# Kernel optimization log

Measured on AMD Instinct MI355X. Metric: run time of the kernel, lower is better.

The kernel has to match this reference:

```python
import jax, jax.numpy as jnp
import numpy as np

E = 8            # num_experts
TOPK = 2
CAP_FACTOR = 1.0
MIN_CAP = 4
AUX_COEF = 0.01


def setup_inputs() -> dict:
    key = jax.random.key(0)
    k1, k2, k3, k4 = jax.random.split(key, 4)
    S, H, F = 2048, 1024, 4096
    return {
        "hidden_states": jax.random.normal(k1, (S, H), dtype=jnp.float32),
        "wg": jax.random.normal(k2, (H, E), dtype=jnp.float32) * 0.02,
        "w1": jax.random.normal(k3, (E, H, F), dtype=jnp.float32) * 0.02,
        "w2": jax.random.normal(k4, (E, F, H), dtype=jnp.float32) * 0.02,
    }


def reference(hidden_states, wg, w1, w2):
    x = hidden_states  # [S, H]
    S, H = x.shape
    capacity = max(int(np.ceil(S * TOPK * CAP_FACTOR / E)), MIN_CAP)  # static

    # ---- top-2 gating (DeepSpeed top2gating) ----
    logits = x @ wg                                   # [S, E]
    gates = jax.nn.softmax(logits, axis=-1)
    idx1 = jnp.argmax(gates, axis=1)
    mask1 = jax.nn.one_hot(idx1, E, dtype=x.dtype)    # [S, E]
    logits_wo1 = jnp.where(mask1 > 0, -jnp.inf, logits)
    idx2 = jnp.argmax(logits_wo1, axis=1)
    mask2 = jax.nn.one_hot(idx2, E, dtype=x.dtype)

    # positions within each expert buffer
    loc1 = jnp.cumsum(mask1, axis=0) - 1.0                      # [S, E]
    loc2 = jnp.cumsum(mask2, axis=0) - 1.0 + jnp.sum(mask1, axis=0, keepdims=True)

    # load-balancing aux loss (computed before capacity drop)
    me = jnp.mean(gates, axis=0)
    ce = jnp.mean(mask1, axis=0)
    l_aux = jnp.mean(me * ce) * E * E * AUX_COEF
    exp_counts = jnp.sum(mask1, axis=0).astype(jnp.int32)

    # drop tokens over capacity
    mask1 = mask1 * (loc1 < capacity).astype(x.dtype)
    mask2 = mask2 * (loc2 < capacity).astype(x.dtype)

    loc1_s = jnp.sum(loc1 * mask1, axis=1).astype(jnp.int32)    # [S]
    loc2_s = jnp.sum(loc2 * mask2, axis=1).astype(jnp.int32)

    gates1_s = jnp.sum(gates * mask1, axis=1)                   # [S]
    gates2_s = jnp.sum(gates * mask2, axis=1)
    denom = jnp.clip(gates1_s + gates2_s, jnp.finfo(x.dtype).eps, None)
    g1 = gates1_s / denom
    g2 = gates2_s / denom

    oh1 = jax.nn.one_hot(loc1_s, capacity, dtype=x.dtype)       # [S, C]
    oh2 = jax.nn.one_hot(loc2_s, capacity, dtype=x.dtype)
    combine = (g1[:, None, None] * mask1[:, :, None] * oh1[:, None, :]
               + g2[:, None, None] * mask2[:, :, None] * oh2[:, None, :])  # [S, E, C]
    dispatch_mask = (combine > 0).astype(x.dtype)

    # ---- dispatch, expert grouped-GEMM (MLP: gelu), combine ----
    dispatched = jnp.einsum("sec,sh->ech", dispatch_mask, x)    # [E, C, H]
    h = jax.nn.gelu(jnp.einsum("ech,ehf->ecf", dispatched, w1))
    expert_out = jnp.einsum("ecf,efh->ech", h, w2)              # [E, C, H]
    output = jnp.einsum("sec,ech->sh", combine, expert_out)     # [S, H]

    return output, l_aux, exp_counts
```

## Files before the change

### kernel.cpp

```cpp
#include <hip/hip_runtime.h>
#include <cstdint>
#include <cstddef>

#define NT 2048
#define HD 1024
#define FD 4096
#define NE 8
#define CAP 512

typedef __bf16 bf16x8_t __attribute__((ext_vector_type(8)));
typedef float f32x4_t __attribute__((ext_vector_type(4)));

typedef const __attribute__((address_space(1))) void* as1_cvp;
typedef __attribute__((address_space(3))) void* as3_vp;

__device__ __forceinline__ void load_lds16(const void* g, void* s) {
  __builtin_amdgcn_global_load_lds((as1_cvp)g, (as3_vp)s, 16, 0, 0);
}

__device__ __forceinline__ unsigned short f2bf(float f) {
  unsigned int u = __float_as_uint(f);
  unsigned int r = (u + 0x7fffu + ((u >> 16) & 1u)) >> 16;
  return (unsigned short)r;
}

__device__ __forceinline__ float gelu_tanh(float x) {
  float inner = 0.7978845608028654f * (x + 0.044715f * x * x * x);
  return 0.5f * x * (1.0f + tanhf(inner));
}

__global__ __launch_bounds__(64) void gating_kernel(
    const float* __restrict__ x, const float* __restrict__ wg,
    float* __restrict__ gates, int* __restrict__ idx1, int* __restrict__ idx2,
    float* __restrict__ gate1, float* __restrict__ gate2)
{
  int s = blockIdx.x;
  int lane = threadIdx.x;
  const float* xs = x + (size_t)s * HD;
  float acc[NE];
  #pragma unroll
  for (int e = 0; e < NE; ++e) acc[e] = 0.f;
  #pragma unroll
  for (int i = 0; i < HD / 64; ++i) {
    int h = i * 64 + lane;
    float xv = xs[h];
    const float4 w0 = *(const float4*)(wg + (size_t)h * NE);
    const float4 w1 = *(const float4*)(wg + (size_t)h * NE + 4);
    acc[0] += xv * w0.x; acc[1] += xv * w0.y; acc[2] += xv * w0.z; acc[3] += xv * w0.w;
    acc[4] += xv * w1.x; acc[5] += xv * w1.y; acc[6] += xv * w1.z; acc[7] += xv * w1.w;
  }
  #pragma unroll
  for (int off = 32; off > 0; off >>= 1) {
    #pragma unroll
    for (int e = 0; e < NE; ++e) acc[e] += __shfl_down(acc[e], off);
  }
  if (lane == 0) {
    float m = acc[0];
    #pragma unroll
    for (int e = 1; e < NE; ++e) m = fmaxf(m, acc[e]);
    float p[NE]; float sum = 0.f;
    #pragma unroll
    for (int e = 0; e < NE; ++e) { p[e] = expf(acc[e] - m); sum += p[e]; }
    float inv = 1.0f / sum;
    int i1 = 0; float b1 = acc[0];
    #pragma unroll
    for (int e = 1; e < NE; ++e) if (acc[e] > b1) { b1 = acc[e]; i1 = e; }
    int i2 = (i1 == 0) ? 1 : 0; float b2 = acc[i2];
    #pragma unroll
    for (int e = 0; e < NE; ++e) if (e != i1 && acc[e] > b2) { b2 = acc[e]; i2 = e; }
    #pragma unroll
    for (int e = 0; e < NE; ++e) gates[(size_t)s * NE + e] = p[e] * inv;
    idx1[s] = i1; idx2[s] = i2;
    gate1[s] = p[i1] * inv;
    gate2[s] = p[i2] * inv;
  }
}

__global__ __launch_bounds__(512) void scan_kernel(
    const int* __restrict__ idx1, const int* __restrict__ idx2,
    const float* __restrict__ gate1, const float* __restrict__ gate2,
    const float* __restrict__ gates,
    int* __restrict__ loc1a, int* __restrict__ loc2a,
    float* __restrict__ g1a, float* __restrict__ g2a,
    int* __restrict__ slot1a, int* __restrict__ slot2a,
    int* __restrict__ slot_tok, float* __restrict__ out_tail)
{
  __shared__ int cnt1[NE];
  __shared__ float gsum[NE];
  int tid = threadIdx.x;
  for (int i = tid; i < NE * CAP; i += 512) slot_tok[i] = -1;
  if (tid < NE) gsum[tid] = 0.f;
  int w = tid >> 6, lane = tid & 63;
  unsigned long long below = (1ull << lane) - 1ull;

  int run = 0;
  for (int c = 0; c < NT / 64; ++c) {
    int s = c * 64 + lane;
    bool m = (idx1[s] == w);
    unsigned long long bal = __ballot(m);
    if (m) loc1a[s] = run + (int)__popcll(bal & below);
    run += (int)__popcll(bal);
  }
  if (lane == 0) cnt1[w] = run;
  int run2 = run;
  for (int c = 0; c < NT / 64; ++c) {
    int s = c * 64 + lane;
    bool m = (idx2[s] == w);
    unsigned long long bal = __ballot(m);
    if (m) loc2a[s] = run2 + (int)__popcll(bal & below);
    run2 += (int)__popcll(bal);
  }
  __syncthreads();

  for (int s = tid; s < NT; s += 512) {
    int e1 = idx1[s], e2 = idx2[s];
    int l1 = loc1a[s], l2 = loc2a[s];
    bool k1 = (l1 < CAP), k2 = (l2 < CAP);
    float g1r = k1 ? gate1[s] : 0.f;
    float g2r = k2 ? gate2[s] : 0.f;
    float denom = fmaxf(g1r + g2r, 1.1920929e-07f);
    g1a[s] = g1r / denom;
    g2a[s] = g2r / denom;
    int s1 = k1 ? (e1 * CAP + l1) : -1;
    int s2 = k2 ? (e2 * CAP + l2) : -1;
    slot1a[s] = s1; slot2a[s] = s2;
    if (s1 >= 0) slot_tok[s1] = s;
    if (s2 >= 0) slot_tok[s2] = s;
  }

  float part[NE];
  #pragma unroll
  for (int e = 0; e < NE; ++e) part[e] = 0.f;
  for (int s = tid; s < NT; s += 512) {
    const float* gr = gates + (size_t)s * NE;
    #pragma unroll
    for (int e = 0; e < NE; ++e) part[e] += gr[e];
  }
  #pragma unroll
  for (int e = 0; e < NE; ++e) atomicAdd(&gsum[e], part[e]);
  __syncthreads();
  if (tid == 0) {
    float laux = 0.f;
    #pragma unroll
    for (int e = 0; e < NE; ++e)
      laux += (gsum[e] / (float)NT) * ((float)cnt1[e] / (float)NT);
    laux *= (float)(NE * NE) * 0.01f;
    out_tail[0] = laux;
  }
  if (tid < NE) out_tail[1 + tid] = (float)cnt1[tid];
}

__global__ __launch_bounds__(256) void transpose_cast_kernel(
    const float* __restrict__ in, unsigned short* __restrict__ out, int K, int N)
{
  __shared__ float tile[64 * 65];
  size_t ebase = (size_t)blockIdx.z * (size_t)K * N;
  const float* ine = in + ebase;
  unsigned short* oute = out + ebase;
  int n0 = blockIdx.x * 64, k0 = blockIdx.y * 64;
  int tid = threadIdx.x;
  #pragma unroll
  for (int i = 0; i < 4; ++i) {
    int chunk = i * 256 + tid;
    int r = chunk >> 4, c = (chunk & 15) * 4;
    float4 v = *(const float4*)(ine + (size_t)(k0 + r) * N + n0 + c);
    tile[r * 65 + c + 0] = v.x;
    tile[r * 65 + c + 1] = v.y;
    tile[r * 65 + c + 2] = v.z;
    tile[r * 65 + c + 3] = v.w;
  }
  __syncthreads();
  #pragma unroll
  for (int i = 0; i < 4; ++i) {
    int chunk = i * 256 + tid;
    int nr = chunk >> 4, kc = (chunk & 15) * 4;
    float a = tile[(kc + 0) * 65 + nr];
    float b = tile[(kc + 1) * 65 + nr];
    float c2 = tile[(kc + 2) * 65 + nr];
    float d = tile[(kc + 3) * 65 + nr];
    uint2 p;
    p.x = (unsigned)f2bf(a) | ((unsigned)f2bf(b) << 16);
    p.y = (unsigned)f2bf(c2) | ((unsigned)f2bf(d) << 16);
    *(uint2*)(oute + (size_t)(n0 + nr) * K + k0 + kc) = p;
  }
}

__global__ __launch_bounds__(64) void gather_kernel(
    const float* __restrict__ x, const int* __restrict__ slot_tok,
    unsigned short* __restrict__ A)
{
  int slot = blockIdx.x;
  int t = slot_tok[slot];
  int tid = threadIdx.x;
  unsigned short* dst = A + (size_t)slot * HD;
  if (t >= 0) {
    const float* src = x + (size_t)t * HD;
    #pragma unroll
    for (int i = 0; i < 4; ++i) {
      int idx = i * 256 + tid * 4;
      float4 v = *(const float4*)(src + idx);
      uint2 p;
      p.x = (unsigned)f2bf(v.x) | ((unsigned)f2bf(v.y) << 16);
      p.y = (unsigned)f2bf(v.z) | ((unsigned)f2bf(v.w) << 16);
      *(uint2*)(dst + idx) = p;
    }
  } else {
    uint2 z; z.x = 0u; z.y = 0u;
    #pragma unroll
    for (int i = 0; i < 4; ++i) {
      int idx = i * 256 + tid * 4;
      *(uint2*)(dst + idx) = z;
    }
  }
}

template <bool FUSE_GELU_BF16>
__global__ __launch_bounds__(256) void gemm_bt_kernel(
    const unsigned short* __restrict__ A, const unsigned short* __restrict__ BT,
    void* __restrict__ Cout, int M, int N, int K)
{
  __shared__ unsigned short As[128 * 32];
  __shared__ unsigned short Bs[128 * 32];
  const int tid = threadIdx.x;
  const int w = tid >> 6, lane = tid & 63;
  const int wm = (w >> 1) * 64, wn = (w & 1) * 64;
  const int quad = lane >> 4, l15 = lane & 15;
  const int m0 = blockIdx.y * 128, n0 = blockIdx.x * 128;
  const size_t e = blockIdx.z;
  const unsigned short* Ae = A + e * (size_t)M * K;
  const unsigned short* Be = BT + e * (size_t)N * K;

  const int lin0 = tid, lin1 = 256 + tid;
  const unsigned short* ga0 = Ae + (size_t)(m0 + (lin0 >> 2)) * K + (lin0 & 3) * 8;
  const unsigned short* ga1 = Ae + (size_t)(m0 + (lin1 >> 2)) * K + (lin1 & 3) * 8;
  const unsigned short* gb0 = Be + (size_t)(n0 + (lin0 >> 2)) * K + (lin0 & 3) * 8;
  const unsigned short* gb1 = Be + (size_t)(n0 + (lin1 >> 2)) * K + (lin1 & 3) * 8;
  char* sa0 = (char*)As + w * 1024;
  char* sa1 = (char*)As + 4096 + w * 1024;
  char* sb0 = (char*)Bs + w * 1024;
  char* sb1 = (char*)Bs + 4096 + w * 1024;

  f32x4_t acc[4][4];
  f32x4_t zz = {0.f, 0.f, 0.f, 0.f};
  #pragma unroll
  for (int mi = 0; mi < 4; ++mi)
    #pragma unroll
    for (int ni = 0; ni < 4; ++ni) acc[mi][ni] = zz;

  const int aoff0 = (wm + l15) * 32 + quad * 8;
  const int boff0 = (wn + l15) * 32 + quad * 8;

  for (int kt = 0; kt < K; kt += 32) {
    load_lds16(ga0, sa0);
    load_lds16(ga1, sa1);
    load_lds16(gb0, sb0);
    load_lds16(gb1, sb1);
    ga0 += 32; ga1 += 32; gb0 += 32; gb1 += 32;
    __syncthreads();
    bf16x8_t af[4], bf[4];
    #pragma unroll
    for (int mi = 0; mi < 4; ++mi)
      af[mi] = *(const bf16x8_t*)(As + aoff0 + mi * 16 * 32);
    #pragma unroll
    for (int ni = 0; ni < 4; ++ni)
      bf[ni] = *(const bf16x8_t*)(Bs + boff0 + ni * 16 * 32);
    #pragma unroll
    for (int mi = 0; mi < 4; ++mi)
      #pragma unroll
      for (int ni = 0; ni < 4; ++ni)
        acc[mi][ni] = __builtin_amdgcn_mfma_f32_16x16x32_bf16(af[mi], bf[ni], acc[mi][ni], 0, 0, 0);
    __syncthreads();
  }

  const size_t cbase = e * (size_t)M * N;
  #pragma unroll
  for (int mi = 0; mi < 4; ++mi) {
    int rowb = m0 + wm + mi * 16 + quad * 4;
    #pragma unroll
    for (int ni = 0; ni < 4; ++ni) {
      int col = n0 + wn + ni * 16 + l15;
      #pragma unroll
      for (int r = 0; r < 4; ++r) {
        float v = acc[mi][ni][r];
        size_t idx = cbase + (size_t)(rowb + r) * N + col;
        if (FUSE_GELU_BF16) {
          ((unsigned short*)Cout)[idx] = f2bf(gelu_tanh(v));
        } else {
          ((float*)Cout)[idx] = v;
        }
      }
    }
  }
}

__global__ __launch_bounds__(64) void combine_kernel(
    const float* __restrict__ eo, const float* __restrict__ g1a,
    const float* __restrict__ g2a, const int* __restrict__ slot1a,
    const int* __restrict__ slot2a, float* __restrict__ out)
{
  int s = blockIdx.x, tid = threadIdx.x;
  float g1 = g1a[s], g2 = g2a[s];
  int s1 = slot1a[s], s2 = slot2a[s];
  float m1 = (s1 < 0) ? 0.f : g1;
  float m2 = (s2 < 0) ? 0.f : g2;
  const float* r1 = eo + (size_t)(s1 < 0 ? 0 : s1) * HD;
  const float* r2 = eo + (size_t)(s2 < 0 ? 0 : s2) * HD;
  #pragma unroll
  for (int i = 0; i < 4; ++i) {
    int idx = i * 256 + tid * 4;
    float4 a = *(const float4*)(r1 + idx);
    float4 b = *(const float4*)(r2 + idx);
    float4 o;
    o.x = m1 * a.x + m2 * b.x;
    o.y = m1 * a.y + m2 * b.y;
    o.z = m1 * a.z + m2 * b.z;
    o.w = m1 * a.w + m2 * b.w;
    *(float4*)(out + (size_t)s * HD + idx) = o;
  }
}

#define OFF_GATES   ((size_t)0)
#define OFF_IDX1    ((size_t)65536)
#define OFF_IDX2    ((size_t)73728)
#define OFF_GATE1   ((size_t)81920)
#define OFF_GATE2   ((size_t)90112)
#define OFF_LOC1    ((size_t)98304)
#define OFF_LOC2    ((size_t)106496)
#define OFF_G1      ((size_t)114688)
#define OFF_G2      ((size_t)122880)
#define OFF_SLOT1   ((size_t)131072)
#define OFF_SLOT2   ((size_t)139264)
#define OFF_SLOTTOK ((size_t)147456)
#define OFF_A       ((size_t)262144)
#define OFF_H       ((size_t)8650752)
#define OFF_W1T     ((size_t)42205184)
#define OFF_W2T     ((size_t)109314048)
#define OFF_EO      ((size_t)176422912)
#define WS_NEEDED   ((size_t)193200128)

extern "C" void kernel_launch(void* const* d_in, const int* in_sizes, int n_in,
                              void* d_out, int out_size, void* d_ws, size_t ws_size,
                              hipStream_t stream) {
  (void)in_sizes; (void)n_in; (void)out_size;
  if (ws_size < WS_NEEDED) return;

  const float* x  = (const float*)d_in[0];
  const float* wg = (const float*)d_in[1];
  const float* w1 = (const float*)d_in[2];
  const float* w2 = (const float*)d_in[3];
  char* ws = (char*)d_ws;
  float* out = (float*)d_out;

  float* gates = (float*)(ws + OFF_GATES);
  int*   idx1  = (int*)(ws + OFF_IDX1);
  int*   idx2  = (int*)(ws + OFF_IDX2);
  float* gate1 = (float*)(ws + OFF_GATE1);
  float* gate2 = (float*)(ws + OFF_GATE2);
  int*   loc1  = (int*)(ws + OFF_LOC1);
  int*   loc2  = (int*)(ws + OFF_LOC2);
  float* g1a   = (float*)(ws + OFF_G1);
  float* g2a   = (float*)(ws + OFF_G2);
  int*   slot1 = (int*)(ws + OFF_SLOT1);
  int*   slot2 = (int*)(ws + OFF_SLOT2);
  int*   stok  = (int*)(ws + OFF_SLOTTOK);
  unsigned short* Abf  = (unsigned short*)(ws + OFF_A);
  unsigned short* hbuf = (unsigned short*)(ws + OFF_H);
  unsigned short* w1t  = (unsigned short*)(ws + OFF_W1T);
  unsigned short* w2t  = (unsigned short*)(ws + OFF_W2T);
  float* eo = (float*)(ws + OFF_EO);

  transpose_cast_kernel<<<dim3(FD / 64, HD / 64, NE), 256, 0, stream>>>(w1, w1t, HD, FD);
  transpose_cast_kernel<<<dim3(HD / 64, FD / 64, NE), 256, 0, stream>>>(w2, w2t, FD, HD);

  gating_kernel<<<NT, 64, 0, stream>>>(x, wg, gates, idx1, idx2, gate1, gate2);
  scan_kernel<<<1, 512, 0, stream>>>(idx1, idx2, gate1, gate2, gates,
                                     loc1, loc2, g1a, g2a, slot1, slot2, stok,
                                     out + (size_t)NT * HD);
  gather_kernel<<<NE * CAP, 64, 0, stream>>>(x, stok, Abf);

  gemm_bt_kernel<true><<<dim3(FD / 128, CAP / 128, NE), 256, 0, stream>>>(
      Abf, w1t, (void*)hbuf, CAP, FD, HD);
  gemm_bt_kernel<false><<<dim3(HD / 128, CAP / 128, NE), 256, 0, stream>>>(
      hbuf, w2t, (void*)eo, CAP, HD, FD);

  combine_kernel<<<NT, 64, 0, stream>>>(eo, g1a, g2a, slot1, slot2, out);
}
```

Before: 545.1 us.

## Fuse weight transpose-cast into GEMMs, split-K second GEMM, faster gelu and gating

Drops the separate transpose/cast kernels for w1 and w2. The GEMMs now read fp32 weights directly, converting them to bf16 and transposing them into LDS on each k-tile. The second GEMM uses 4-way split-K, writing partial sums that the combine kernel adds up, which raises the block count from 256 to 1024. Gelu is replaced by an exp2/rcp sigmoid form, the gating kernel packs 4 tokens per block, and the scan kernel caches indices in LDS and reduces with shuffles before the atomics. Trade-offs: each GEMM block now does strided uncoalesced-per-thread fp32 weight loads and conversion work inline without async LDS loads, and split-K adds partial-buffer traffic.

```diff
diff --git a/kernel.cpp b/kernel.cpp
--- a/kernel.cpp
+++ b/kernel.cpp
@@ -7,6 +7,9 @@
 #define FD 4096
 #define NE 8
 #define CAP 512
+#define KSPLIT 4
+
+#define BROW 40
 
 typedef __bf16 bf16x8_t __attribute__((ext_vector_type(8)));
 typedef float f32x4_t __attribute__((ext_vector_type(4)));
@@ -24,18 +27,19 @@
   return (unsigned short)r;
 }
 
-__device__ __forceinline__ float gelu_tanh(float x) {
-  float inner = 0.7978845608028654f * (x + 0.044715f * x * x * x);
-  return 0.5f * x * (1.0f + tanhf(inner));
-}
-
-__global__ __launch_bounds__(64) void gating_kernel(
+__device__ __forceinline__ float gelu_fast(float x) {
+  float u = x + 0.044715f * x * x * x;
+  float t = __builtin_amdgcn_exp2f(-2.3022077f * u);
+  return x * __builtin_amdgcn_rcpf(1.0f + t);
+}
+
+__global__ __launch_bounds__(256) void gating_kernel(
     const float* __restrict__ x, const float* __restrict__ wg,
     float* __restrict__ gates, int* __restrict__ idx1, int* __restrict__ idx2,
     float* __restrict__ gate1, float* __restrict__ gate2)
 {
-  int s = blockIdx.x;
-  int lane = threadIdx.x;
+  int s = blockIdx.x * 4 + (threadIdx.x >> 6);
+  int lane = threadIdx.x & 63;
   const float* xs = x + (size_t)s * HD;
   float acc[NE];
   #pragma unroll
@@ -87,16 +91,20 @@
 {
   __shared__ int cnt1[NE];
   __shared__ float gsum[NE];
+  __shared__ int i1s[NT];
+  __shared__ int i2s[NT];
   int tid = threadIdx.x;
   for (int i = tid; i < NE * CAP; i += 512) slot_tok[i] = -1;
+  for (int i = tid; i < NT; i += 512) { i1s[i] = idx1[i]; i2s[i] = idx2[i]; }
   if (tid < NE) gsum[tid] = 0.f;
+  __syncthreads();
   int w = tid >> 6, lane = tid & 63;
   unsigned long long below = (1ull << lane) - 1ull;
 
   int run = 0;
   for (int c = 0; c < NT / 64; ++c) {
     int s = c * 64 + lane;
-    bool m = (idx1[s] == w);
+    bool m = (i1s[s] == w);
     unsigned long long bal = __ballot(m);
     if (m) loc1a[s] = run + (int)__popcll(bal & below);
     run += (int)__popcll(bal);
@@ -105,7 +113,7 @@
   int run2 = run;
   for (int c = 0; c < NT / 64; ++c) {
     int s = c * 64 + lane;
-    bool m = (idx2[s] == w);
+    bool m = (i2s[s] == w);
     unsigned long long bal = __ballot(m);
     if (m) loc2a[s] = run2 + (int)__popcll(bal & below);
     run2 += (int)__popcll(bal);
@@ -113,7 +121,7 @@
   __syncthreads();
 
   for (int s = tid; s < NT; s += 512) {
-    int e1 = idx1[s], e2 = idx2[s];
+    int e1 = i1s[s], e2 = i2s[s];
     int l1 = loc1a[s], l2 = loc2a[s];
     bool k1 = (l1 < CAP), k2 = (l2 < CAP);
     float g1r = k1 ? gate1[s] : 0.f;
@@ -137,7 +145,14 @@
     for (int e = 0; e < NE; ++e) part[e] += gr[e];
   }
   #pragma unroll
-  for (int e = 0; e < NE; ++e) atomicAdd(&gsum[e], part[e]);
+  for (int off = 32; off > 0; off >>= 1) {
+    #pragma unroll
+    for (int e = 0; e < NE; ++e) part[e] += __shfl_down(part[e], off);
+  }
+  if (lane == 0) {
+    #pragma unroll
+    for (int e = 0; e < NE; ++e) atomicAdd(&gsum[e], part[e]);
+  }
   __syncthreads();
   if (tid == 0) {
     float laux = 0.f;
@@ -148,41 +163,6 @@
     out_tail[0] = laux;
   }
   if (tid < NE) out_tail[1 + tid] = (float)cnt1[tid];
-}
-
-__global__ __launch_bounds__(256) void transpose_cast_kernel(
-    const float* __restrict__ in, unsigned short* __restrict__ out, int K, int N)
-{
-  __shared__ float tile[64 * 65];
-  size_t ebase = (size_t)blockIdx.z * (size_t)K * N;
-  const float* ine = in + ebase;
-  unsigned short* oute = out + ebase;
-  int n0 = blockIdx.x * 64, k0 = blockIdx.y * 64;
-  int tid = threadIdx.x;
-  #pragma unroll
-  for (int i = 0; i < 4; ++i) {
-    int chunk = i * 256 + tid;
-    int r = chunk >> 4, c = (chunk & 15) * 4;
-    float4 v = *(const float4*)(ine + (size_t)(k0 + r) * N + n0 + c);
-    tile[r * 65 + c + 0] = v.x;
-    tile[r * 65 + c + 1] = v.y;
-    tile[r * 65 + c + 2] = v.z;
-    tile[r * 65 + c + 3] = v.w;
-  }
-  __syncthreads();
-  #pragma unroll
-  for (int i = 0; i < 4; ++i) {
-    int chunk = i * 256 + tid;
-    int nr = chunk >> 4, kc = (chunk & 15) * 4;
-    float a = tile[(kc + 0) * 65 + nr];
-    float b = tile[(kc + 1) * 65 + nr];
-    float c2 = tile[(kc + 2) * 65 + nr];
-    float d = tile[(kc + 3) * 65 + nr];
-    uint2 p;
-    p.x = (unsigned)f2bf(a) | ((unsigned)f2bf(b) << 16);
-    p.y = (unsigned)f2bf(c2) | ((unsigned)f2bf(d) << 16);
-    *(uint2*)(oute + (size_t)(n0 + nr) * K + k0 + kc) = p;
-  }
 }
 
 __global__ __launch_bounds__(64) void gather_kernel(
@@ -214,31 +194,39 @@
   }
 }
 
-template <bool FUSE_GELU_BF16>
-__global__ __launch_bounds__(256) void gemm_bt_kernel(
-    const unsigned short* __restrict__ A, const unsigned short* __restrict__ BT,
+template <bool SPLITK, bool GELU>
+__global__ __launch_bounds__(256) void gemm_fused_kernel(
+    const unsigned short* __restrict__ A, const float* __restrict__ W,
     void* __restrict__ Cout, int M, int N, int K)
 {
   __shared__ unsigned short As[128 * 32];
-  __shared__ unsigned short Bs[128 * 32];
+  __shared__ unsigned short Bs[128 * BROW];
   const int tid = threadIdx.x;
   const int w = tid >> 6, lane = tid & 63;
   const int wm = (w >> 1) * 64, wn = (w & 1) * 64;
   const int quad = lane >> 4, l15 = lane & 15;
   const int m0 = blockIdx.y * 128, n0 = blockIdx.x * 128;
-  const size_t e = blockIdx.z;
-  const unsigned short* Ae = A + e * (size_t)M * K;
-  const unsigned short* Be = BT + e * (size_t)N * K;
+
+  size_t e; int sk, klen, kb;
+  if (SPLITK) { e = blockIdx.z >> 2; sk = blockIdx.z & 3; klen = K / KSPLIT; kb = sk * klen; }
+  else        { e = blockIdx.z;      sk = 0;              klen = K;          kb = 0; }
+
+  const unsigned short* Ae = A + e * (size_t)M * K + kb;
+  const float* We = W + e * (size_t)K * N + (size_t)kb * N + n0;
 
   const int lin0 = tid, lin1 = 256 + tid;
   const unsigned short* ga0 = Ae + (size_t)(m0 + (lin0 >> 2)) * K + (lin0 & 3) * 8;
   const unsigned short* ga1 = Ae + (size_t)(m0 + (lin1 >> 2)) * K + (lin1 & 3) * 8;
-  const unsigned short* gb0 = Be + (size_t)(n0 + (lin0 >> 2)) * K + (lin0 & 3) * 8;
-  const unsigned short* gb1 = Be + (size_t)(n0 + (lin1 >> 2)) * K + (lin1 & 3) * 8;
   char* sa0 = (char*)As + w * 1024;
   char* sa1 = (char*)As + 4096 + w * 1024;
-  char* sb0 = (char*)Bs + w * 1024;
-  char* sb1 = (char*)Bs + 4096 + w * 1024;
+
+  const int bn = tid & 127;
+  const int oct0 = tid >> 7;
+  const int oct1 = oct0 + 2;
+  const float* gw0 = We + (size_t)(oct0 * 8) * N + bn;
+  const float* gw1 = We + (size_t)(oct1 * 8) * N + bn;
+  unsigned short* bs0 = Bs + bn * BROW + oct0 * 8;
+  unsigned short* bs1 = Bs + bn * BROW + oct1 * 8;
 
   f32x4_t acc[4][4];
   f32x4_t zz = {0.f, 0.f, 0.f, 0.f};
@@ -248,14 +236,27 @@
     for (int ni = 0; ni < 4; ++ni) acc[mi][ni] = zz;
 
   const int aoff0 = (wm + l15) * 32 + quad * 8;
-  const int boff0 = (wn + l15) * 32 + quad * 8;
-
-  for (int kt = 0; kt < K; kt += 32) {
+  const int boff0 = (wn + l15) * BROW + quad * 8;
+
+  for (int kt = 0; kt < klen; kt += 32) {
     load_lds16(ga0, sa0);
     load_lds16(ga1, sa1);
-    load_lds16(gb0, sb0);
-    load_lds16(gb1, sb1);
-    ga0 += 32; ga1 += 32; gb0 += 32; gb1 += 32;
+    ga0 += 32; ga1 += 32;
+    float b0[8], b1[8];
+    #pragma unroll
+    for (int j = 0; j < 8; ++j) { b0[j] = gw0[(size_t)j * N]; b1[j] = gw1[(size_t)j * N]; }
+    gw0 += (size_t)32 * N; gw1 += (size_t)32 * N;
+    uint4 p0, p1;
+    p0.x = (unsigned)f2bf(b0[0]) | ((unsigned)f2bf(b0[1]) << 16);
+    p0.y = (unsigned)f2bf(b0[2]) | ((unsigned)f2bf(b0[3]) << 16);
+    p0.z = (unsigned)f2bf(b0[4]) | ((unsigned)f2bf(b0[5]) << 16);
+    p0.w = (unsigned)f2bf(b0[6]) | ((unsigned)f2bf(b0[7]) << 16);
+    p1.x = (unsigned)f2bf(b1[0]) | ((unsigned)f2bf(b1[1]) << 16);
+    p1.y = (unsigned)f2bf(b1[2]) | ((unsigned)f2bf(b1[3]) << 16);
+    p1.z = (unsigned)f2bf(b1[4]) | ((unsigned)f2bf(b1[5]) << 16);
+    p1.w = (unsigned)f2bf(b1[6]) | ((unsigned)f2bf(b1[7]) << 16);
+    *(uint4*)bs0 = p0;
+    *(uint4*)bs1 = p1;
     __syncthreads();
     bf16x8_t af[4], bf[4];
     #pragma unroll
@@ -263,7 +264,7 @@
       af[mi] = *(const bf16x8_t*)(As + aoff0 + mi * 16 * 32);
     #pragma unroll
     for (int ni = 0; ni < 4; ++ni)
-      bf[ni] = *(const bf16x8_t*)(Bs + boff0 + ni * 16 * 32);
+      bf[ni] = *(const bf16x8_t*)(Bs + boff0 + ni * 16 * BROW);
     #pragma unroll
     for (int mi = 0; mi < 4; ++mi)
       #pragma unroll
@@ -272,7 +273,6 @@
     __syncthreads();
   }
 
-  const size_t cbase = e * (size_t)M * N;
   #pragma unroll
   for (int mi = 0; mi < 4; ++mi) {
     int rowb = m0 + wm + mi * 16 + quad * 4;
@@ -282,10 +282,11 @@
       #pragma unroll
       for (int r = 0; r < 4; ++r) {
         float v = acc[mi][ni][r];
-        size_t idx = cbase + (size_t)(rowb + r) * N + col;
-        if (FUSE_GELU_BF16) {
-          ((unsigned short*)Cout)[idx] = f2bf(gelu_tanh(v));
+        if (GELU) {
+          size_t idx = e * (size_t)M * N + (size_t)(rowb + r) * N + col;
+          ((unsigned short*)Cout)[idx] = f2bf(gelu_fast(v));
         } else {
+          size_t idx = ((size_t)sk * NE + e) * (size_t)M * N + (size_t)(rowb + r) * N + col;
           ((float*)Cout)[idx] = v;
         }
       }
@@ -294,7 +295,7 @@
 }
 
 __global__ __launch_bounds__(64) void combine_kernel(
-    const float* __restrict__ eo, const float* __restrict__ g1a,
+    const float* __restrict__ eop, const float* __restrict__ g1a,
     const float* __restrict__ g2a, const int* __restrict__ slot1a,
     const int* __restrict__ slot2a, float* __restrict__ out)
 {
@@ -303,18 +304,26 @@
   int s1 = slot1a[s], s2 = slot2a[s];
   float m1 = (s1 < 0) ? 0.f : g1;
   float m2 = (s2 < 0) ? 0.f : g2;
-  const float* r1 = eo + (size_t)(s1 < 0 ? 0 : s1) * HD;
-  const float* r2 = eo + (size_t)(s2 < 0 ? 0 : s2) * HD;
+  const float* r1 = eop + (size_t)(s1 < 0 ? 0 : s1) * HD;
+  const float* r2 = eop + (size_t)(s2 < 0 ? 0 : s2) * HD;
+  const size_t PSTRIDE = (size_t)NE * CAP * HD;
   #pragma unroll
   for (int i = 0; i < 4; ++i) {
     int idx = i * 256 + tid * 4;
-    float4 a = *(const float4*)(r1 + idx);
-    float4 b = *(const float4*)(r2 + idx);
+    float ax = 0.f, ay = 0.f, az = 0.f, aw = 0.f;
+    float bx = 0.f, by = 0.f, bz = 0.f, bw = 0.f;
+    #pragma unroll
+    for (int p = 0; p < KSPLIT; ++p) {
+      float4 a = *(const float4*)(r1 + p * PSTRIDE + idx);
+      float4 b = *(const float4*)(r2 + p * PSTRIDE + idx);
+      ax += a.x; ay += a.y; az += a.z; aw += a.w;
+      bx += b.x; by += b.y; bz += b.z; bw += b.w;
+    }
     float4 o;
-    o.x = m1 * a.x + m2 * b.x;
-    o.y = m1 * a.y + m2 * b.y;
-    o.z = m1 * a.z + m2 * b.z;
-    o.w = m1 * a.w + m2 * b.w;
+    o.x = m1 * ax + m2 * bx;
+    o.y = m1 * ay + m2 * by;
+    o.z = m1 * az + m2 * bz;
+    o.w = m1 * aw + m2 * bw;
     *(float4*)(out + (size_t)s * HD + idx) = o;
   }
 }
@@ -333,10 +342,8 @@
 #define OFF_SLOTTOK ((size_t)147456)
 #define OFF_A       ((size_t)262144)
 #define OFF_H       ((size_t)8650752)
-#define OFF_W1T     ((size_t)42205184)
-#define OFF_W2T     ((size_t)109314048)
-#define OFF_EO      ((size_t)176422912)
-#define WS_NEEDED   ((size_t)193200128)
+#define OFF_EOPART  ((size_t)42205184)
+#define WS_NEEDED   ((size_t)109314048)
 
 extern "C" void kernel_launch(void* const* d_in, const int* in_sizes, int n_in,
                               void* d_out, int out_size, void* d_ws, size_t ws_size,
@@ -365,23 +372,18 @@
   int*   stok  = (int*)(ws + OFF_SLOTTOK);
   unsigned short* Abf  = (unsigned short*)(ws + OFF_A);
   unsigned short* hbuf = (unsigned short*)(ws + OFF_H);
-  unsigned short* w1t  = (unsigned short*)(ws + OFF_W1T);
-  unsigned short* w2t  = (unsigned short*)(ws + OFF_W2T);
-  float* eo = (float*)(ws + OFF_EO);
-
-  transpose_cast_kernel<<<dim3(FD / 64, HD / 64, NE), 256, 0, stream>>>(w1, w1t, HD, FD);
-  transpose_cast_kernel<<<dim3(HD / 64, FD / 64, NE), 256, 0, stream>>>(w2, w2t, FD, HD);
-
-  gating_kernel<<<NT, 64, 0, stream>>>(x, wg, gates, idx1, idx2, gate1, gate2);
+  float* eopart = (float*)(ws + OFF_EOPART);
+
+  gating_kernel<<<NT / 4, 256, 0, stream>>>(x, wg, gates, idx1, idx2, gate1, gate2);
   scan_kernel<<<1, 512, 0, stream>>>(idx1, idx2, gate1, gate2, gates,
                                      loc1, loc2, g1a, g2a, slot1, slot2, stok,
                                      out + (size_t)NT * HD);
   gather_kernel<<<NE * CAP, 64, 0, stream>>>(x, stok, Abf);
 
-  gemm_bt_kernel<true><<<dim3(FD / 128, CAP / 128, NE), 256, 0, stream>>>(
-      Abf, w1t, (void*)hbuf, CAP, FD, HD);
-  gemm_bt_kernel<false><<<dim3(HD / 128, CAP / 128, NE), 256, 0, stream>>>(
-      hbuf, w2t, (void*)eo, CAP, HD, FD);
-
-  combine_kernel<<<NT, 64, 0, stream>>>(eo, g1a, g2a, slot1, slot2, out);
-}
+  gemm_fused_kernel<false, true><<<dim3(FD / 128, CAP / 128, NE), 256, 0, stream>>>(
+      Abf, w1, (void*)hbuf, CAP, FD, HD);
+  gemm_fused_kernel<true, false><<<dim3(HD / 128, CAP / 128, NE * KSPLIT), 256, 0, stream>>>(
+      hbuf, w2, (void*)eopart, CAP, HD, FD);
+
+  combine_kernel<<<NT, 64, 0, stream>>>(eopart, g1a, g2a, slot1, slot2, out);
+}
```

New measurement: 450.7 us. 1.21x faster.
